# Kernel tuning notes

Measured on AMD Instinct MI355X. Metric: run time of the kernel, lower is better.

## Reference

```python
import jax, jax.numpy as jnp
import numpy as np

MARGIN = 0.3

def setup_inputs() -> dict:
    key = jax.random.key(0)
    k1, k2 = jax.random.split(key)
    z1 = jax.random.normal(k1, (8192, 128), dtype=jnp.float32)
    z2 = jax.random.normal(k2, (8192, 128), dtype=jnp.float32)
    return {"z1": z1, "z2": z2}

def _cdist(z1, z2):
    # Euclidean pairwise distances via the GEMM identity, avoiding the
    # [N, N, d] broadcasted intermediate. Clamp for numerical safety.
    sq1 = jnp.sum(z1 * z1, axis=1, keepdims=True)        # [N, 1]
    sq2 = jnp.sum(z2 * z2, axis=1, keepdims=True).T      # [1, N]
    d2 = sq1 + sq2 - 2.0 * (z1 @ z2.T)                   # [N, N]
    return jnp.sqrt(jnp.maximum(d2, 0.0))

def reference(z1, z2) -> jnp.ndarray:
    n = z1.shape[0]
    dist = _cdist(z1, z2)                                # [N, N]
    pos_dist = jnp.diagonal(dist)                        # [N]
    # hard negative mining: mask diagonal with +inf, take row-min
    eye = jnp.eye(n, dtype=bool)
    neg_dist = jnp.where(eye, jnp.inf, dist)
    hard_neg = jnp.min(neg_dist, axis=1)                 # [N]
    loss = jax.nn.relu(pos_dist - hard_neg + MARGIN)
    return jnp.mean(loss)
```

## Files before the change

kernel.cpp:

```cpp
#include <hip/hip_runtime.h>

#define MARGIN 0.3f

typedef __attribute__((ext_vector_type(8))) short short8;
typedef __attribute__((ext_vector_type(4))) float floatx4;


__device__ __forceinline__ unsigned enc_f32(float f) {
    unsigned u = __float_as_uint(f);
    return (u & 0x80000000u) ? ~u : (u | 0x80000000u);
}
__device__ __forceinline__ float dec_f32(unsigned u) {
    return (u & 0x80000000u) ? __uint_as_float(u & 0x7fffffffu)
                             : __uint_as_float(~u);
}
__device__ __forceinline__ short f2bf(float f) {
    unsigned u = __float_as_uint(f);
    u = u + 0x7fffu + ((u >> 16) & 1u);
    return (short)(u >> 16);
}

__global__ void init_kernel(unsigned* __restrict__ rowmin, unsigned* __restrict__ cnt,
                            float* __restrict__ out) {
    int i = blockIdx.x * 512 + threadIdx.x;
    rowmin[i] = 0xFFFFFFFFu;
    if (blockIdx.x == 0) {
        if (threadIdx.x < 32) cnt[threadIdx.x] = 0u;
        if (threadIdx.x == 0) out[0] = 0.0f;
    }
}

__global__ __launch_bounds__(512, 2)
void fused_kernel(const float* __restrict__ z1, const float* __restrict__ z2,
                  float* __restrict__ posd,
                  unsigned* __restrict__ rowmin, unsigned* __restrict__ cnt,
                  float* __restrict__ out, int n)
{
    __shared__ __align__(16) short bt[65536];
    __shared__ __align__(16) float s2l[512];
    __shared__ __align__(16) float sq1l[512];
    __shared__ float lsum[8];
    __shared__ int   fin_s;

    const int bid = blockIdx.x;
    const int xcd = bid & 7, idx = bid >> 3;
    const int rg  = (xcd << 1) | (idx >> 4);
    const int cgi = idx & 15;

    const int tid = threadIdx.x, w = tid >> 6, lane = tid & 63;
    const int quad = lane >> 4, l15 = lane & 15;
    const int rowbase = rg * 512 + w * 64;
    const int colorig = cgi * 512;

    {
        const float4* zb = (const float4*)(z2 + (size_t)(colorig + tid) * 128);
        float s2 = 0.f;
        #pragma unroll
        for (int kk = 0; kk < 4; ++kk) {
            float4 f[8];
            #pragma unroll
            for (int j = 0; j < 8; ++j) f[j] = zb[kk * 8 + j];
            #pragma unroll
            for (int j = 0; j < 8; ++j)
                s2 += f[j].x*f[j].x + f[j].y*f[j].y + f[j].z*f[j].z + f[j].w*f[j].w;
            #pragma unroll
            for (int q = 0; q < 4; ++q) {
                float4 a = f[q * 2], b = f[q * 2 + 1];
                short8 sc = { f2bf(-2.f*a.x), f2bf(-2.f*a.y), f2bf(-2.f*a.z), f2bf(-2.f*a.w),
                              f2bf(-2.f*b.x), f2bf(-2.f*b.y), f2bf(-2.f*b.z), f2bf(-2.f*b.w) };
                *(short8*)&bt[(tid >> 4) * 2048 + kk * 512 + q * 128 + (tid & 15) * 8] = sc;
            }
        }
        s2l[tid] = s2;
    }

    short8 af[4][4];
    {
        float s1p[4] = {0.f, 0.f, 0.f, 0.f};
        #pragma unroll
        for (int sm = 0; sm < 4; ++sm) {
            const float4* zr = (const float4*)(z1 + (size_t)(rowbase + sm * 16 + l15) * 128);
            #pragma unroll
            for (int kk = 0; kk < 4; ++kk) {
                float4 u0 = zr[kk * 8 + quad * 2];
                float4 u1 = zr[kk * 8 + quad * 2 + 1];
                s1p[sm] += u0.x*u0.x + u0.y*u0.y + u0.z*u0.z + u0.w*u0.w
                         + u1.x*u1.x + u1.y*u1.y + u1.z*u1.z + u1.w*u1.w;
                af[sm][kk] = { f2bf(u0.x), f2bf(u0.y), f2bf(u0.z), f2bf(u0.w),
                               f2bf(u1.x), f2bf(u1.y), f2bf(u1.z), f2bf(u1.w) };
            }
        }
        #pragma unroll
        for (int sm = 0; sm < 4; ++sm) {
            float s1 = s1p[sm];
            s1 += __shfl_xor(s1, 16);
            s1 += __shfl_xor(s1, 32);
            if (quad == 0) sq1l[w * 64 + sm * 16 + l15] = s1;
        }
    }

    {
        int ri = rg * 512 + cgi * 32 + (tid >> 4);
        int e  = (tid & 15) * 8;
        const float4* p1 = (const float4*)(z1 + (size_t)ri * 128 + e);
        const float4* p2 = (const float4*)(z2 + (size_t)ri * 128 + e);
        float4 a0 = p1[0], a1 = p1[1], b0 = p2[0], b1 = p2[1];
        float dx0 = a0.x-b0.x, dy0 = a0.y-b0.y, dz0 = a0.z-b0.z, dw0 = a0.w-b0.w;
        float dx1 = a1.x-b1.x, dy1 = a1.y-b1.y, dz1 = a1.z-b1.z, dw1 = a1.w-b1.w;
        float p2a = dx0*dx0 + dy0*dy0 + dz0*dz0 + dw0*dw0
                  + dx1*dx1 + dy1*dy1 + dz1*dz1 + dw1*dw1;
        #pragma unroll
        for (int m = 8; m >= 1; m >>= 1) p2a += __shfl_xor(p2a, m);
        if ((tid & 15) == 0) posd[ri] = sqrtf(p2a);
    }

    __syncthreads();

    float vmin[4][4];
    #pragma unroll
    for (int sm = 0; sm < 4; ++sm)
        #pragma unroll
        for (int reg = 0; reg < 4; ++reg)
            vmin[sm][reg] = 3.0e38f;

    #pragma unroll
    for (int S = 0; S < 8; ++S) {
        const short* bs_ = &bt[S * 8192];
        #pragma unroll
        for (int hf = 0; hf < 2; ++hf) {
            const int tcol = S * 64 + hf * 32;
            const int colbase = colorig + tcol;
            const float s2v0 = s2l[tcol + l15];
            const float s2v1 = s2l[tcol + 16 + l15];

            short8 bq[2][4];
            #pragma unroll
            for (int sn = 0; sn < 2; ++sn)
                #pragma unroll
                for (int kk = 0; kk < 4; ++kk)
                    bq[sn][kk] = *(const short8*)(bs_ + hf * 4096 + sn * 2048
                                                  + kk * 512 + lane * 8);

            floatx4 acc[4][2];
            #pragma unroll
            for (int sm = 0; sm < 4; ++sm)
                #pragma unroll
                for (int reg = 0; reg < 4; ++reg) {
                    acc[sm][0][reg] = s2v0;
                    acc[sm][1][reg] = s2v1;
                }

            __builtin_amdgcn_s_setprio(1);
            #pragma unroll
            for (int kk = 0; kk < 4; ++kk)
                #pragma unroll
                for (int sm = 0; sm < 4; ++sm)
                    #pragma unroll
                    for (int sn = 0; sn < 2; ++sn)
                        acc[sm][sn] = __builtin_amdgcn_mfma_f32_16x16x32_bf16(
                            af[sm][kk], bq[sn][kk], acc[sm][sn], 0, 0, 0);
            __builtin_amdgcn_s_setprio(0);

            if (colbase < rowbase + 64 && rowbase < colbase + 32) {
                #pragma unroll
                for (int sm = 0; sm < 4; ++sm)
                    #pragma unroll
                    for (int reg = 0; reg < 4; ++reg) {
                        int gi = rowbase + sm * 16 + quad * 4 + reg;
                        float v0 = acc[sm][0][reg];
                        float v1 = acc[sm][1][reg];
                        v0 = (gi == colbase + l15)      ? 3.0e38f : v0;
                        v1 = (gi == colbase + 16 + l15) ? 3.0e38f : v1;
                        vmin[sm][reg] = fminf(vmin[sm][reg], fminf(v0, v1));
                    }
            } else {
                #pragma unroll
                for (int sm = 0; sm < 4; ++sm)
                    #pragma unroll
                    for (int reg = 0; reg < 4; ++reg)
                        vmin[sm][reg] = fminf(vmin[sm][reg],
                            fminf(acc[sm][0][reg], acc[sm][1][reg]));
            }
        }
    }

    #pragma unroll
    for (int sm = 0; sm < 4; ++sm)
        #pragma unroll
        for (int reg = 0; reg < 4; ++reg) {
            float vm = vmin[sm][reg];
            #pragma unroll
            for (int m = 8; m >= 1; m >>= 1)
                vm = fminf(vm, __shfl_xor(vm, m));
            if (l15 == 0)
                atomicMin(&rowmin[rowbase + sm * 16 + quad * 4 + reg], enc_f32(vm));
        }

    __syncthreads();
    if (tid == 0) {
        __threadfence();
        fin_s = (atomicAdd(&cnt[rg], 1u) == 15u);
    }
    __syncthreads();
    if (!fin_s) return;
    __threadfence();

    {
        int i = rg * 512 + tid;
        unsigned rm = atomicMin(&rowmin[i], 0xFFFFFFFFu);
        float hard = sqrtf(fmaxf(sq1l[tid] + dec_f32(rm), 0.0f));
        float l = fmaxf(posd[i] - hard + MARGIN, 0.0f);
        #pragma unroll
        for (int m = 32; m >= 1; m >>= 1) l += __shfl_xor(l, m);
        if (lane == 0) lsum[w] = l;
    }
    __syncthreads();
    if (tid == 0) {
        float t = 0.f;
        #pragma unroll
        for (int i = 0; i < 8; ++i) t += lsum[i];
        atomicAdd(out, t / (float)n);
    }
}

extern "C" void kernel_launch(void* const* d_in, const int* in_sizes, int n_in,
                              void* d_out, int out_size, void* d_ws, size_t ws_size,
                              hipStream_t stream) {
    const float* z1 = (const float*)d_in[0];
    const float* z2 = (const float*)d_in[1];
    const int n = in_sizes[0] / 128;

    char* ws = (char*)d_ws;
    float*    posd   = (float*)ws;
    unsigned* rowmin = (unsigned*)(ws + (size_t)n * 4);
    unsigned* cnt    = (unsigned*)(ws + (size_t)n * 8);
    float*    out    = (float*)d_out;

    init_kernel<<<n / 512, 512, 0, stream>>>(rowmin, cnt, out);
    fused_kernel<<<(n / 512) * (n / 512), 512, 0, stream>>>(
        z1, z2, posd, rowmin, cnt, out, n);
}
```

Measured before the change: 96.30 us.

## Switch to 32x32x16 MFMA tiles and replace atomic rowmin with per-column-group buffer

```diff
diff --git a/kernel.cpp b/kernel.cpp
--- a/kernel.cpp
+++ b/kernel.cpp
@@ -3,37 +3,19 @@
 #define MARGIN 0.3f
 
 typedef __attribute__((ext_vector_type(8))) short short8;
-typedef __attribute__((ext_vector_type(4))) float floatx4;
-
-
-__device__ __forceinline__ unsigned enc_f32(float f) {
-    unsigned u = __float_as_uint(f);
-    return (u & 0x80000000u) ? ~u : (u | 0x80000000u);
-}
-__device__ __forceinline__ float dec_f32(unsigned u) {
-    return (u & 0x80000000u) ? __uint_as_float(u & 0x7fffffffu)
-                             : __uint_as_float(~u);
-}
+typedef __attribute__((ext_vector_type(16))) float floatx16;
+
+
 __device__ __forceinline__ short f2bf(float f) {
     unsigned u = __float_as_uint(f);
     u = u + 0x7fffu + ((u >> 16) & 1u);
     return (short)(u >> 16);
 }
 
-__global__ void init_kernel(unsigned* __restrict__ rowmin, unsigned* __restrict__ cnt,
-                            float* __restrict__ out) {
-    int i = blockIdx.x * 512 + threadIdx.x;
-    rowmin[i] = 0xFFFFFFFFu;
-    if (blockIdx.x == 0) {
-        if (threadIdx.x < 32) cnt[threadIdx.x] = 0u;
-        if (threadIdx.x == 0) out[0] = 0.0f;
-    }
-}
-
-__global__ __launch_bounds__(512, 2)
+__global__ __launch_bounds__(512, 1)
 void fused_kernel(const float* __restrict__ z1, const float* __restrict__ z2,
-                  float* __restrict__ posd,
-                  unsigned* __restrict__ rowmin, unsigned* __restrict__ cnt,
+                  float* __restrict__ rowmin2d, float* __restrict__ posd,
+                  float* __restrict__ psum, unsigned* __restrict__ cnt,
                   float* __restrict__ out, int n)
 {
     __shared__ __align__(16) short bt[65536];
@@ -48,7 +30,7 @@
     const int cgi = idx & 15;
 
     const int tid = threadIdx.x, w = tid >> 6, lane = tid & 63;
-    const int quad = lane >> 4, l15 = lane & 15;
+    const int l31 = lane & 31, hi = lane >> 5;
     const int rowbase = rg * 512 + w * 64;
     const int colorig = cgi * 512;
 
@@ -74,29 +56,22 @@
         s2l[tid] = s2;
     }
 
-    short8 af[4][4];
-    {
-        float s1p[4] = {0.f, 0.f, 0.f, 0.f};
-        #pragma unroll
-        for (int sm = 0; sm < 4; ++sm) {
-            const float4* zr = (const float4*)(z1 + (size_t)(rowbase + sm * 16 + l15) * 128);
-            #pragma unroll
-            for (int kk = 0; kk < 4; ++kk) {
-                float4 u0 = zr[kk * 8 + quad * 2];
-                float4 u1 = zr[kk * 8 + quad * 2 + 1];
-                s1p[sm] += u0.x*u0.x + u0.y*u0.y + u0.z*u0.z + u0.w*u0.w
-                         + u1.x*u1.x + u1.y*u1.y + u1.z*u1.z + u1.w*u1.w;
-                af[sm][kk] = { f2bf(u0.x), f2bf(u0.y), f2bf(u0.z), f2bf(u0.w),
-                               f2bf(u1.x), f2bf(u1.y), f2bf(u1.z), f2bf(u1.w) };
-            }
-        }
-        #pragma unroll
-        for (int sm = 0; sm < 4; ++sm) {
-            float s1 = s1p[sm];
-            s1 += __shfl_xor(s1, 16);
-            s1 += __shfl_xor(s1, 32);
-            if (quad == 0) sq1l[w * 64 + sm * 16 + l15] = s1;
-        }
+    short8 af[2][8];
+    #pragma unroll
+    for (int rb = 0; rb < 2; ++rb) {
+        const float4* zr = (const float4*)(z1 + (size_t)(rowbase + rb * 32 + l31) * 128);
+        float s1p = 0.f;
+        #pragma unroll
+        for (int kk16 = 0; kk16 < 8; ++kk16) {
+            float4 u0 = zr[kk16 * 4 + hi * 2];
+            float4 u1 = zr[kk16 * 4 + hi * 2 + 1];
+            s1p += u0.x*u0.x + u0.y*u0.y + u0.z*u0.z + u0.w*u0.w
+                 + u1.x*u1.x + u1.y*u1.y + u1.z*u1.z + u1.w*u1.w;
+            af[rb][kk16] = { f2bf(u0.x), f2bf(u0.y), f2bf(u0.z), f2bf(u0.w),
+                             f2bf(u1.x), f2bf(u1.y), f2bf(u1.z), f2bf(u1.w) };
+        }
+        float s1 = s1p + __shfl_xor(s1p, 32);
+        if (hi == 0) sq1l[w * 64 + rb * 32 + l31] = s1;
     }
 
     {
@@ -116,84 +91,66 @@
 
     __syncthreads();
 
-    float vmin[4][4];
-    #pragma unroll
-    for (int sm = 0; sm < 4; ++sm)
-        #pragma unroll
-        for (int reg = 0; reg < 4; ++reg)
-            vmin[sm][reg] = 3.0e38f;
+    const int lofs = ((lane >> 4) & 1) * 2048 + hi * 128 + (lane & 15) * 8;
+
+    float vmin[2][16];
+    #pragma unroll
+    for (int rb = 0; rb < 2; ++rb)
+        #pragma unroll
+        for (int r = 0; r < 16; ++r)
+            vmin[rb][r] = 3.0e38f;
 
     #pragma unroll
     for (int S = 0; S < 8; ++S) {
-        const short* bs_ = &bt[S * 8192];
-        #pragma unroll
-        for (int hf = 0; hf < 2; ++hf) {
-            const int tcol = S * 64 + hf * 32;
-            const int colbase = colorig + tcol;
-            const float s2v0 = s2l[tcol + l15];
-            const float s2v1 = s2l[tcol + 16 + l15];
-
-            short8 bq[2][4];
-            #pragma unroll
-            for (int sn = 0; sn < 2; ++sn)
+        const short* bs_ = &bt[S * 8192] + lofs;
+        #pragma unroll
+        for (int cb = 0; cb < 2; ++cb) {
+            const float s2v = s2l[S * 64 + cb * 32 + l31];
+            const short* base = bs_ + cb * 4096;
+
+            floatx16 a0, a1;
+            #pragma unroll
+            for (int r = 0; r < 16; ++r) { a0[r] = s2v; a1[r] = s2v; }
+
+            #pragma unroll
+            for (int kk16 = 0; kk16 < 8; ++kk16) {
+                short8 b = *(const short8*)(base + (kk16 >> 1) * 512 + (kk16 & 1) * 256);
+                a0 = __builtin_amdgcn_mfma_f32_32x32x16_bf16(af[0][kk16], b, a0, 0, 0, 0);
+                a1 = __builtin_amdgcn_mfma_f32_32x32x16_bf16(af[1][kk16], b, a1, 0, 0, 0);
+            }
+
+            const int cbcol = colorig + S * 64 + cb * 32;
+            if (cbcol < rowbase + 64 && rowbase < cbcol + 32) {
                 #pragma unroll
-                for (int kk = 0; kk < 4; ++kk)
-                    bq[sn][kk] = *(const short8*)(bs_ + hf * 4096 + sn * 2048
-                                                  + kk * 512 + lane * 8);
-
-            floatx4 acc[4][2];
-            #pragma unroll
-            for (int sm = 0; sm < 4; ++sm)
-                #pragma unroll
-                for (int reg = 0; reg < 4; ++reg) {
-                    acc[sm][0][reg] = s2v0;
-                    acc[sm][1][reg] = s2v1;
+                for (int r = 0; r < 16; ++r) {
+                    int gr = (r & 3) + 8 * (r >> 2) + 4 * hi;
+                    int gi0 = rowbase + gr, gi1 = rowbase + 32 + gr;
+                    float v0 = (gi0 == cbcol + l31) ? 3.0e38f : a0[r];
+                    float v1 = (gi1 == cbcol + l31) ? 3.0e38f : a1[r];
+                    vmin[0][r] = fminf(vmin[0][r], v0);
+                    vmin[1][r] = fminf(vmin[1][r], v1);
                 }
-
-            __builtin_amdgcn_s_setprio(1);
-            #pragma unroll
-            for (int kk = 0; kk < 4; ++kk)
-                #pragma unroll
-                for (int sm = 0; sm < 4; ++sm)
-                    #pragma unroll
-                    for (int sn = 0; sn < 2; ++sn)
-                        acc[sm][sn] = __builtin_amdgcn_mfma_f32_16x16x32_bf16(
-                            af[sm][kk], bq[sn][kk], acc[sm][sn], 0, 0, 0);
-            __builtin_amdgcn_s_setprio(0);
-
-            if (colbase < rowbase + 64 && rowbase < colbase + 32) {
-                #pragma unroll
-                for (int sm = 0; sm < 4; ++sm)
-                    #pragma unroll
-                    for (int reg = 0; reg < 4; ++reg) {
-                        int gi = rowbase + sm * 16 + quad * 4 + reg;
-                        float v0 = acc[sm][0][reg];
-                        float v1 = acc[sm][1][reg];
-                        v0 = (gi == colbase + l15)      ? 3.0e38f : v0;
-                        v1 = (gi == colbase + 16 + l15) ? 3.0e38f : v1;
-                        vmin[sm][reg] = fminf(vmin[sm][reg], fminf(v0, v1));
-                    }
             } else {
                 #pragma unroll
-                for (int sm = 0; sm < 4; ++sm)
-                    #pragma unroll
-                    for (int reg = 0; reg < 4; ++reg)
-                        vmin[sm][reg] = fminf(vmin[sm][reg],
-                            fminf(acc[sm][0][reg], acc[sm][1][reg]));
+                for (int r = 0; r < 16; ++r) {
+                    vmin[0][r] = fminf(vmin[0][r], a0[r]);
+                    vmin[1][r] = fminf(vmin[1][r], a1[r]);
+                }
             }
         }
     }
 
     #pragma unroll
-    for (int sm = 0; sm < 4; ++sm)
-        #pragma unroll
-        for (int reg = 0; reg < 4; ++reg) {
-            float vm = vmin[sm][reg];
-            #pragma unroll
-            for (int m = 8; m >= 1; m >>= 1)
+    for (int rb = 0; rb < 2; ++rb)
+        #pragma unroll
+        for (int r = 0; r < 16; ++r) {
+            float vm = vmin[rb][r];
+            #pragma unroll
+            for (int m = 16; m >= 1; m >>= 1)
                 vm = fminf(vm, __shfl_xor(vm, m));
-            if (l15 == 0)
-                atomicMin(&rowmin[rowbase + sm * 16 + quad * 4 + reg], enc_f32(vm));
+            if (l31 == 0)
+                rowmin2d[(size_t)cgi * n + rowbase + rb * 32
+                         + (r & 3) + 8 * (r >> 2) + 4 * hi] = vm;
         }
 
     __syncthreads();
@@ -207,8 +164,11 @@
 
     {
         int i = rg * 512 + tid;
-        unsigned rm = atomicMin(&rowmin[i], 0xFFFFFFFFu);
-        float hard = sqrtf(fmaxf(sq1l[tid] + dec_f32(rm), 0.0f));
+        float mn = rowmin2d[i];
+        #pragma unroll
+        for (int c = 1; c < 16; ++c)
+            mn = fminf(mn, rowmin2d[(size_t)c * n + i]);
+        float hard = sqrtf(fmaxf(sq1l[tid] + mn, 0.0f));
         float l = fmaxf(posd[i] - hard + MARGIN, 0.0f);
         #pragma unroll
         for (int m = 32; m >= 1; m >>= 1) l += __shfl_xor(l, m);
@@ -219,7 +179,16 @@
         float t = 0.f;
         #pragma unroll
         for (int i = 0; i < 8; ++i) t += lsum[i];
-        atomicAdd(out, t / (float)n);
+        atomicExch(&psum[rg], t);
+        __threadfence();
+        if (atomicAdd(&cnt[16], 1u) == 15u) {
+            __threadfence();
+            float tot = 0.f;
+            #pragma unroll
+            for (int j = 0; j < 16; ++j)
+                tot += atomicAdd(&psum[j], 0.0f);
+            out[0] = tot / (float)n;
+        }
     }
 }
 
@@ -231,12 +200,13 @@
     const int n = in_sizes[0] / 128;
 
     char* ws = (char*)d_ws;
-    float*    posd   = (float*)ws;
-    unsigned* rowmin = (unsigned*)(ws + (size_t)n * 4);
-    unsigned* cnt    = (unsigned*)(ws + (size_t)n * 8);
-    float*    out    = (float*)d_out;
-
-    init_kernel<<<n / 512, 512, 0, stream>>>(rowmin, cnt, out);
+    float*    rowmin2d = (float*)ws;
+    float*    posd     = (float*)(ws + (size_t)16 * n * 4);
+    float*    psum     = (float*)(ws + (size_t)17 * n * 4);
+    unsigned* cnt      = (unsigned*)(ws + (size_t)17 * n * 4 + 256);
+    float*    out      = (float*)d_out;
+
+    hipMemsetAsync(cnt, 0, 128, stream);
     fused_kernel<<<(n / 512) * (n / 512), 512, 0, stream>>>(
-        z1, z2, posd, rowmin, cnt, out, n);
+        z1, z2, rowmin2d, posd, psum, cnt, out, n);
 }
```

Measured after the change: 116.6 us. +21.0%, slower.

## Replace atomic row-min with per-colgroup partial buffer and hardware bf16 pack

Applied to the files above, without the earlier changes.

```diff
diff --git a/kernel.cpp b/kernel.cpp
--- a/kernel.cpp
+++ b/kernel.cpp
@@ -4,36 +4,29 @@
 
 typedef __attribute__((ext_vector_type(8))) short short8;
 typedef __attribute__((ext_vector_type(4))) float floatx4;
-
-
-__device__ __forceinline__ unsigned enc_f32(float f) {
-    unsigned u = __float_as_uint(f);
-    return (u & 0x80000000u) ? ~u : (u | 0x80000000u);
-}
-__device__ __forceinline__ float dec_f32(unsigned u) {
-    return (u & 0x80000000u) ? __uint_as_float(u & 0x7fffffffu)
-                             : __uint_as_float(~u);
-}
-__device__ __forceinline__ short f2bf(float f) {
-    unsigned u = __float_as_uint(f);
-    u = u + 0x7fffu + ((u >> 16) & 1u);
-    return (short)(u >> 16);
-}
-
-__global__ void init_kernel(unsigned* __restrict__ rowmin, unsigned* __restrict__ cnt,
-                            float* __restrict__ out) {
-    int i = blockIdx.x * 512 + threadIdx.x;
-    rowmin[i] = 0xFFFFFFFFu;
-    if (blockIdx.x == 0) {
-        if (threadIdx.x < 32) cnt[threadIdx.x] = 0u;
-        if (threadIdx.x == 0) out[0] = 0.0f;
-    }
+typedef __attribute__((ext_vector_type(4))) unsigned uintx4;
+
+
+__device__ __forceinline__ unsigned cvt_pk(float a, float b) {
+    unsigned r;
+    asm("v_cvt_pk_bf16_f32 %0, %1, %2" : "=v"(r) : "v"(a), "v"(b));
+    return r;
+}
+__device__ __forceinline__ unsigned cvt_pk_neg(float a, float b) {
+    unsigned r;
+    asm("v_cvt_pk_bf16_f32 %0, -%1, -%2" : "=v"(r) : "v"(a), "v"(b));
+    return r;
+}
+__device__ __forceinline__ short8 make8(unsigned p0, unsigned p1,
+                                        unsigned p2, unsigned p3) {
+    uintx4 u = { p0, p1, p2, p3 };
+    return __builtin_bit_cast(short8, u);
 }
 
 __global__ __launch_bounds__(512, 2)
 void fused_kernel(const float* __restrict__ z1, const float* __restrict__ z2,
-                  float* __restrict__ posd,
-                  unsigned* __restrict__ rowmin, unsigned* __restrict__ cnt,
+                  float* __restrict__ rowmin2d, float* __restrict__ posd,
+                  float* __restrict__ psum, unsigned* __restrict__ cnt,
                   float* __restrict__ out, int n)
 {
     __shared__ __align__(16) short bt[65536];
@@ -66,12 +59,12 @@
             #pragma unroll
             for (int q = 0; q < 4; ++q) {
                 float4 a = f[q * 2], b = f[q * 2 + 1];
-                short8 sc = { f2bf(-2.f*a.x), f2bf(-2.f*a.y), f2bf(-2.f*a.z), f2bf(-2.f*a.w),
-                              f2bf(-2.f*b.x), f2bf(-2.f*b.y), f2bf(-2.f*b.z), f2bf(-2.f*b.w) };
-                *(short8*)&bt[(tid >> 4) * 2048 + kk * 512 + q * 128 + (tid & 15) * 8] = sc;
+                uintx4 sc = { cvt_pk_neg(a.x, a.y), cvt_pk_neg(a.z, a.w),
+                              cvt_pk_neg(b.x, b.y), cvt_pk_neg(b.z, b.w) };
+                *(uintx4*)&bt[(tid >> 4) * 2048 + kk * 512 + q * 128 + (tid & 15) * 8] = sc;
             }
         }
-        s2l[tid] = s2;
+        s2l[tid] = 0.5f * s2;
     }
 
     short8 af[4][4];
@@ -86,8 +79,8 @@
                 float4 u1 = zr[kk * 8 + quad * 2 + 1];
                 s1p[sm] += u0.x*u0.x + u0.y*u0.y + u0.z*u0.z + u0.w*u0.w
                          + u1.x*u1.x + u1.y*u1.y + u1.z*u1.z + u1.w*u1.w;
-                af[sm][kk] = { f2bf(u0.x), f2bf(u0.y), f2bf(u0.z), f2bf(u0.w),
-                               f2bf(u1.x), f2bf(u1.y), f2bf(u1.z), f2bf(u1.w) };
+                af[sm][kk] = make8(cvt_pk(u0.x, u0.y), cvt_pk(u0.z, u0.w),
+                                   cvt_pk(u1.x, u1.y), cvt_pk(u1.z, u1.w));
             }
         }
         #pragma unroll
@@ -193,7 +186,7 @@
             for (int m = 8; m >= 1; m >>= 1)
                 vm = fminf(vm, __shfl_xor(vm, m));
             if (l15 == 0)
-                atomicMin(&rowmin[rowbase + sm * 16 + quad * 4 + reg], enc_f32(vm));
+                rowmin2d[(size_t)cgi * n + rowbase + sm * 16 + quad * 4 + reg] = vm;
         }
 
     __syncthreads();
@@ -207,8 +200,11 @@
 
     {
         int i = rg * 512 + tid;
-        unsigned rm = atomicMin(&rowmin[i], 0xFFFFFFFFu);
-        float hard = sqrtf(fmaxf(sq1l[tid] + dec_f32(rm), 0.0f));
+        float mn = rowmin2d[i];
+        #pragma unroll
+        for (int c = 1; c < 16; ++c)
+            mn = fminf(mn, rowmin2d[(size_t)c * n + i]);
+        float hard = sqrtf(fmaxf(fmaf(2.0f, mn, sq1l[tid]), 0.0f));
         float l = fmaxf(posd[i] - hard + MARGIN, 0.0f);
         #pragma unroll
         for (int m = 32; m >= 1; m >>= 1) l += __shfl_xor(l, m);
@@ -219,7 +215,16 @@
         float t = 0.f;
         #pragma unroll
         for (int i = 0; i < 8; ++i) t += lsum[i];
-        atomicAdd(out, t / (float)n);
+        atomicExch(&psum[rg], t);
+        __threadfence();
+        if (atomicAdd(&cnt[16], 1u) == 15u) {
+            __threadfence();
+            float tot = 0.f;
+            #pragma unroll
+            for (int j = 0; j < 16; ++j)
+                tot += atomicAdd(&psum[j], 0.0f);
+            out[0] = tot / (float)n;
+        }
     }
 }
 
@@ -231,12 +236,13 @@
     const int n = in_sizes[0] / 128;
 
     char* ws = (char*)d_ws;
-    float*    posd   = (float*)ws;
-    unsigned* rowmin = (unsigned*)(ws + (size_t)n * 4);
-    unsigned* cnt    = (unsigned*)(ws + (size_t)n * 8);
-    float*    out    = (float*)d_out;
-
-    init_kernel<<<n / 512, 512, 0, stream>>>(rowmin, cnt, out);
+    float*    rowmin2d = (float*)ws;
+    float*    posd     = (float*)(ws + (size_t)16 * n * 4);
+    float*    psum     = (float*)(ws + (size_t)17 * n * 4);
+    unsigned* cnt      = (unsigned*)(ws + (size_t)17 * n * 4 + 256);
+    float*    out      = (float*)d_out;
+
+    hipMemsetAsync(cnt, 0, 128, stream);
     fused_kernel<<<(n / 512) * (n / 512), 512, 0, stream>>>(
-        z1, z2, posd, rowmin, cnt, out, n);
-}
+        z1, z2, rowmin2d, posd, psum, cnt, out, n);
+}
```

Result: slower. 102.1 us (+6.1%).
